# Kernel optimization log

Hardware: AMD Instinct MI355X
Metric: run time of the kernel (lower is better)

## Reference

```python
import jax, jax.numpy as jnp
import numpy as np

N_HEAD = 16
N_KV_HEAD = 8
HEAD_DIM = 128
N_EMBED = 2048
EPS = 1.1920929e-07  # torch default eps for fp32 rms_norm


def _apply_rotary_emb(x, cos, sin):
    # x: (B, T, H, D); cos/sin: (1, T, 1, D//2)  (nanochat-style half rotation)
    d = x.shape[-1] // 2
    x1, x2 = x[..., :d], x[..., d:]
    y1 = x1 * cos + x2 * sin
    y2 = -x1 * sin + x2 * cos
    return jnp.concatenate([y1, y2], axis=-1).astype(x.dtype)


def _rms_norm(x):
    return x * jax.lax.rsqrt(jnp.mean(jnp.square(x), axis=-1, keepdims=True) + EPS)


def setup_inputs() -> dict:
    key = jax.random.key(0)
    ks = jax.random.split(key, 5)
    B, T = 2, 2048
    kv_dim = N_KV_HEAD * HEAD_DIM
    x = jax.random.normal(ks[0], (B, T, N_EMBED), dtype=jnp.float32)
    w_attn = jax.random.normal(ks[1], (N_EMBED + 2 * kv_dim, N_EMBED), dtype=jnp.float32) * 0.02
    w_proj = jax.random.normal(ks[2], (N_EMBED, N_EMBED), dtype=jnp.float32) * 0.02
    # realistic RoPE tables
    half = HEAD_DIM // 2
    inv_freq = 1.0 / (10000.0 ** (jnp.arange(half, dtype=jnp.float32) / half))
    freqs = jnp.arange(T, dtype=jnp.float32)[:, None] * inv_freq[None, :]  # (T, half)
    cos = jnp.cos(freqs)[None, :, None, :]
    sin = jnp.sin(freqs)[None, :, None, :]
    return {"x": x, "w_attn": w_attn, "w_proj": w_proj, "cos": cos, "sin": sin}


def reference(x, w_attn, w_proj, cos, sin):
    B, T, C = x.shape
    kv_dim = N_KV_HEAD * HEAD_DIM
    qkv = jnp.einsum('btc,oc->bto', x, w_attn)  # (B, T, C + 2*kv_dim)
    q = qkv[..., :C].reshape(B, T, N_HEAD, HEAD_DIM)
    k = qkv[..., C:C + kv_dim].reshape(B, T, N_KV_HEAD, HEAD_DIM)
    v = qkv[..., C + kv_dim:].reshape(B, T, N_KV_HEAD, HEAD_DIM)
    q = _rms_norm(_apply_rotary_emb(q, cos, sin))
    k = _rms_norm(_apply_rotary_emb(k, cos, sin))
    # GQA: repeat kv heads to match query heads
    rep = N_HEAD // N_KV_HEAD
    k = jnp.repeat(k, rep, axis=2)  # (B, T, n_head, D)
    v = jnp.repeat(v, rep, axis=2)
    scale = 1.0 / jnp.sqrt(jnp.float32(HEAD_DIM))
    scores = jnp.einsum('bqhd,bkhd->bhqk', q, k) * scale  # (B, H, T, T)
    causal = jnp.tril(jnp.ones((T, T), dtype=bool))
    scores = jnp.where(causal[None, None], scores, jnp.finfo(scores.dtype).min)
    attn = jax.nn.softmax(scores, axis=-1)
    y = jnp.einsum('bhqk,bkhd->bqhd', attn, v).reshape(B, T, C)
    return jnp.einsum('btc,oc->bto', y, w_proj)
```

## Files before the change

### kernel.cpp

```cpp
#include <hip/hip_runtime.h>

#define B_ 2
#define T_ 2048
#define NH 16
#define NKV 8
#define HD 128
#define C_ 2048
#define KVD (NKV*HD)
#define QKVD (C_ + 2*KVD)
#define NTOK (B_*T_)

typedef __bf16 bf16_t;
typedef __bf16 bf16x4_t __attribute__((ext_vector_type(4)));
typedef __bf16 bf16x8_t __attribute__((ext_vector_type(8)));
typedef float f32x4_t __attribute__((ext_vector_type(4)));

__device__ __forceinline__ f32x4_t mfma16(bf16x8_t a, bf16x8_t b, f32x4_t c) {
  return __builtin_amdgcn_mfma_f32_16x16x32_bf16(a, b, c, 0, 0, 0);
}

#define GLDS16(gp, lp) __builtin_amdgcn_global_load_lds( \
    (const __attribute__((address_space(1))) void*)(gp), \
    (__attribute__((address_space(3))) void*)(lp), 16, 0, 0)

__global__ __launch_bounds__(256) void cvt_kernel(const float* __restrict__ src,
                                                  bf16_t* __restrict__ dst, int n) {
  int i = (blockIdx.x * 256 + threadIdx.x) * 4;
  if (i >= n) return;
  const float4 v = *(const float4*)(src + i);
  bf16x4_t o;
  o[0] = (bf16_t)v.x; o[1] = (bf16_t)v.y; o[2] = (bf16_t)v.z; o[3] = (bf16_t)v.w;
  *(bf16x4_t*)(dst + i) = o;
}

__global__ void gemm_nt(const bf16_t* __restrict__ A, const bf16_t* __restrict__ Bm,
                        float* __restrict__ C, int M, int N, int K) {
  __shared__ bf16_t As[128*32];
  __shared__ bf16_t Bs[128*32];
  int tid = threadIdx.x;
  int wave = tid >> 6, lane = tid & 63;
  int quad = lane >> 4, l16 = lane & 15;
  int wm = (wave >> 1) * 64, wn = (wave & 1) * 64;
  int bm = blockIdx.y * 128, bn = blockIdx.x * 128;
  int grow = wave * 32 + (lane >> 2);
  int gcol = (lane & 3) * 8;
  const bf16_t* pa = A + (size_t)(bm + grow) * K + gcol;
  const bf16_t* pb = Bm + (size_t)(bn + grow) * K + gcol;
  bf16_t* lA0 = &As[(wave * 32) * 32];
  bf16_t* lA1 = &As[(wave * 32 + 16) * 32];
  bf16_t* lB0 = &Bs[(wave * 32) * 32];
  bf16_t* lB1 = &Bs[(wave * 32 + 16) * 32];
  f32x4_t acc[4][4];
  #pragma unroll
  for (int i = 0; i < 4; i++)
    #pragma unroll
    for (int j = 0; j < 4; j++) acc[i][j] = (f32x4_t){0.f,0.f,0.f,0.f};
  for (int k0 = 0; k0 < K; k0 += 32) {
    __syncthreads();
    GLDS16(pa + k0, lA0);
    GLDS16(pa + (size_t)16 * K + k0, lA1);
    GLDS16(pb + k0, lB0);
    GLDS16(pb + (size_t)16 * K + k0, lB1);
    __syncthreads();
    bf16x8_t af[4], bfr[4];
    #pragma unroll
    for (int i = 0; i < 4; i++) {
      af[i]  = *(const bf16x8_t*)&As[(wm + i*16 + l16)*32 + quad*8];
      bfr[i] = *(const bf16x8_t*)&Bs[(wn + i*16 + l16)*32 + quad*8];
    }
    #pragma unroll
    for (int i = 0; i < 4; i++)
      #pragma unroll
      for (int j = 0; j < 4; j++)
        acc[i][j] = mfma16(af[i], bfr[j], acc[i][j]);
  }
  #pragma unroll
  for (int i = 0; i < 4; i++)
    #pragma unroll
    for (int j = 0; j < 4; j++) {
      int row0 = bm + wm + i*16 + quad*4;
      int col  = bn + wn + j*16 + l16;
      #pragma unroll
      for (int r = 0; r < 4; r++)
        C[(size_t)(row0 + r) * N + col] = acc[i][j][r];
    }
}

__global__ __launch_bounds__(256) void rope_norm_kernel(const float* __restrict__ qkv,
    const float* __restrict__ cosb, const float* __restrict__ sinb,
    bf16_t* __restrict__ qb, bf16_t* __restrict__ kb) {
  int token = blockIdx.y;
  int slot = blockIdx.x * 4 + (threadIdx.x >> 6);
  int lane = threadIdx.x & 63;
  int b = token >> 11, s = token & 2047;
  const float* row = qkv + (size_t)token * QKVD;
  int base_in = (slot < 16) ? slot * HD : C_ + (slot - 16) * HD;
  float x1 = row[base_in + lane];
  float x2 = row[base_in + 64 + lane];
  float c = cosb[s*64 + lane], sn = sinb[s*64 + lane];
  float y1 = x1*c + x2*sn;
  float y2 = x2*c - x1*sn;
  float ss = y1*y1 + y2*y2;
  ss += __shfl_xor(ss, 1);  ss += __shfl_xor(ss, 2);  ss += __shfl_xor(ss, 4);
  ss += __shfl_xor(ss, 8);  ss += __shfl_xor(ss, 16); ss += __shfl_xor(ss, 32);
  float r = rsqrtf(ss * (1.0f/128.0f) + 1.1920929e-07f);
  bf16_t* dst;
  if (slot < 16) {
    r *= 0.08838834764831845f * 1.4426950408889634f;
    dst = qb + ((size_t)(b*NH + slot) * T_ + s) * HD;
  } else {
    dst = kb + ((size_t)(b*NKV + (slot-16)) * T_ + s) * HD;
  }
  dst[lane]      = (bf16_t)(y1 * r);
  dst[lane + 64] = (bf16_t)(y2 * r);
}

__global__ __launch_bounds__(256) void transpose_v(const float* __restrict__ qkv,
                                                   bf16_t* __restrict__ vt) {
  __shared__ bf16_t TT[64*136];
  int bk = blockIdx.y;
  int b = bk >> 3, kv = bk & 7;
  int s0 = blockIdx.x * 64;
  int tid = threadIdx.x;
  int row = tid >> 2, c0 = (tid & 3) * 32;
  const float* src = qkv + (size_t)(b*T_ + s0 + row) * QKVD + C_ + KVD + kv*HD + c0;
  #pragma unroll
  for (int s4 = 0; s4 < 8; s4++) {
    float4 v = *(const float4*)(src + s4*4);
    bf16x4_t pk;
    pk[0] = (bf16_t)v.x; pk[1] = (bf16_t)v.y; pk[2] = (bf16_t)v.z; pk[3] = (bf16_t)v.w;
    *(bf16x4_t*)&TT[row*136 + c0 + s4*4] = pk;
  }
  __syncthreads();
  #pragma unroll
  for (int s2 = 0; s2 < 2; s2++) {
    int d = (tid >> 2) + s2*64;
    #pragma unroll
    for (int s = 0; s < 2; s++) {
      int g = (tid & 3) * 8 + s*32;
      bf16x8_t pk;
      #pragma unroll
      for (int e = 0; e < 8; e++) pk[e] = TT[(g + e)*136 + d];
      *(bf16x8_t*)(vt + ((size_t)bk * HD + d) * T_ + s0 + g) = pk;
    }
  }
}

__global__ __launch_bounds__(256, 2) void attn_kernel(const bf16_t* __restrict__ qb,
    const bf16_t* __restrict__ kb, const bf16_t* __restrict__ vt, bf16_t* __restrict__ yb) {
  __shared__ bf16_t Ks[64*136];
  __shared__ bf16_t Vs[128*72];
  __shared__ bf16_t Ps[4][16*72];
  int bh = blockIdx.y;
  int b = bh >> 4, h = bh & 15, kvh = h >> 1;
  int j = blockIdx.x;
  int tid = threadIdx.x, wave = tid >> 6, lane = tid & 63, quad = lane >> 4, l16 = lane & 15;
  const bf16_t* Qp = qb + (size_t)bh * T_ * HD;
  const bf16_t* Kp = kb + (size_t)(b*NKV + kvh) * T_ * HD;
  const bf16_t* Vt = vt + (size_t)(b*NKV + kvh) * HD * T_;

  int krow = tid >> 2, kc0 = (tid & 3) * 8;
  int vd = tid >> 1,  vc0 = (tid & 1) * 8;

  for (int ph = 0; ph < 2; ph++) {
    int qt = ph ? (31 - j) : j;
    int q0w = qt * 64 + wave * 16;
    bf16x8_t qf[4];
    #pragma unroll
    for (int kc = 0; kc < 4; kc++)
      qf[kc] = *(const bf16x8_t*)(Qp + (size_t)(q0w + l16) * HD + kc*32 + quad*8);

    float mrow = -1e30f, lrow = 0.f;
    f32x4_t o[8];
    #pragma unroll
    for (int mb = 0; mb < 8; mb++) o[mb] = (f32x4_t){0.f,0.f,0.f,0.f};

    int nkt = qt + 1;
    for (int kt = 0; kt < nkt; kt++) {
      int k0 = kt * 64;
      __syncthreads();
      {
        const bf16_t* src = Kp + (size_t)(k0 + krow) * HD + kc0;
        #pragma unroll
        for (int s = 0; s < 4; s++)
          *(bf16x8_t*)&Ks[krow*136 + kc0 + s*32] = *(const bf16x8_t*)(src + s*32);
      }
      {
        const bf16_t* src = Vt + (size_t)vd * T_ + k0 + vc0;
        #pragma unroll
        for (int s = 0; s < 4; s++)
          *(bf16x8_t*)&Vs[vd*72 + vc0 + s*16] = *(const bf16x8_t*)(src + s*16);
      }
      __syncthreads();

      f32x4_t sacc[4];
      #pragma unroll
      for (int mb = 0; mb < 4; mb++) sacc[mb] = (f32x4_t){0.f,0.f,0.f,0.f};
      #pragma unroll
      for (int mb = 0; mb < 4; mb++)
        #pragma unroll
        for (int kc = 0; kc < 4; kc++) {
          bf16x8_t kf = *(const bf16x8_t*)&Ks[(mb*16 + l16)*136 + kc*32 + quad*8];
          sacc[mb] = mfma16(kf, qf[kc], sacc[mb]);
        }
      if (kt == qt) {
        int rowl = wave*16 + l16;
        #pragma unroll
        for (int mb = 0; mb < 4; mb++)
          #pragma unroll
          for (int r = 0; r < 4; r++)
            if (mb*16 + quad*4 + r > rowl) sacc[mb][r] = -1e30f;
      }
      float mx = -1e30f;
      #pragma unroll
      for (int mb = 0; mb < 4; mb++)
        #pragma unroll
        for (int r = 0; r < 4; r++) mx = fmaxf(mx, sacc[mb][r]);
      mx = fmaxf(mx, __shfl_xor(mx, 16));
      mx = fmaxf(mx, __shfl_xor(mx, 32));
      float mnew = fmaxf(mrow, mx);
      float alpha = exp2f(mrow - mnew);
      mrow = mnew;
      float rs = 0.f;
      #pragma unroll
      for (int mb = 0; mb < 4; mb++)
        #pragma unroll
        for (int r = 0; r < 4; r++) {
          float p = exp2f(sacc[mb][r] - mnew);
          sacc[mb][r] = p;
          rs += p;
        }
      rs += __shfl_xor(rs, 16);
      rs += __shfl_xor(rs, 32);
      lrow = lrow * alpha + rs;
      #pragma unroll
      for (int mb = 0; mb < 8; mb++) o[mb] *= alpha;
      #pragma unroll
      for (int mb = 0; mb < 4; mb++) {
        bf16x4_t pk;
        pk[0] = (bf16_t)sacc[mb][0]; pk[1] = (bf16_t)sacc[mb][1];
        pk[2] = (bf16_t)sacc[mb][2]; pk[3] = (bf16_t)sacc[mb][3];
        *(bf16x4_t*)&Ps[wave][l16*72 + mb*16 + quad*4] = pk;
      }
      bf16x8_t pf[2];
      #pragma unroll
      for (int kc = 0; kc < 2; kc++)
        pf[kc] = *(const bf16x8_t*)&Ps[wave][l16*72 + kc*32 + quad*8];
      #pragma unroll
      for (int mb = 0; mb < 8; mb++)
        #pragma unroll
        for (int kc = 0; kc < 2; kc++) {
          bf16x8_t vf = *(const bf16x8_t*)&Vs[(mb*16 + l16)*72 + kc*32 + quad*8];
          o[mb] = mfma16(vf, pf[kc], o[mb]);
        }
    }
    __syncthreads();
    bf16_t* OLw = &Ks[wave * 2176];
    float invl = 1.0f / lrow;
    #pragma unroll
    for (int mb = 0; mb < 8; mb++) {
      bf16x4_t pk;
      pk[0] = (bf16_t)(o[mb][0] * invl); pk[1] = (bf16_t)(o[mb][1] * invl);
      pk[2] = (bf16_t)(o[mb][2] * invl); pk[3] = (bf16_t)(o[mb][3] * invl);
      *(bf16x4_t*)&OLw[l16*136 + mb*16 + quad*4] = pk;
    }
    int row = lane & 15, part = lane >> 4;
    int tok = qt*64 + wave*16 + row;
    bf16_t* dst = yb + ((size_t)(b*T_ + tok) * NH + h) * HD + part*32;
    #pragma unroll
    for (int jj = 0; jj < 4; jj++)
      *(bf16x8_t*)(dst + jj*8) = *(const bf16x8_t*)&OLw[row*136 + part*32 + jj*8];
  }
}

extern "C" void kernel_launch(void* const* d_in, const int* in_sizes, int n_in,
                              void* d_out, int out_size, void* d_ws, size_t ws_size,
                              hipStream_t stream) {
  const float* x      = (const float*)d_in[0];
  const float* w_attn = (const float*)d_in[1];
  const float* w_proj = (const float*)d_in[2];
  const float* cosb   = (const float*)d_in[3];
  const float* sinb   = (const float*)d_in[4];
  float* out = (float*)d_out;

  bf16_t* xb  = (bf16_t*)d_ws;
  bf16_t* wab = xb + 8388608;
  bf16_t* wpb = wab + 8388608;
  float*  qkv = (float*)(wpb + 4194304);
  bf16_t* qb  = (bf16_t*)(qkv + 16777216);
  bf16_t* kb  = qb + 8388608;
  bf16_t* vt  = kb + 4194304;
  bf16_t* yb  = vt + 4194304;

  cvt_kernel<<<8192, 256, 0, stream>>>(x, xb, 8388608);
  cvt_kernel<<<8192, 256, 0, stream>>>(w_attn, wab, 8388608);
  cvt_kernel<<<4096, 256, 0, stream>>>(w_proj, wpb, 4194304);

  gemm_nt<<<dim3(32, 32), 256, 0, stream>>>(xb, wab, qkv, NTOK, QKVD, C_);

  rope_norm_kernel<<<dim3(6, 4096), 256, 0, stream>>>(qkv, cosb, sinb, qb, kb);
  transpose_v<<<dim3(32, 16), 256, 0, stream>>>(qkv, vt);

  attn_kernel<<<dim3(16, 32), 256, 0, stream>>>(qb, kb, vt, yb);

  gemm_nt<<<dim3(16, 32), 256, 0, stream>>>(yb, wpb, out, NTOK, C_, C_);
}
```

Before: 359.6 us.

## Use 32x32 MFMA with 128-row query tiles, bf16 QKV output, and fused conversions

```diff
diff --git a/kernel.cpp b/kernel.cpp
--- a/kernel.cpp
+++ b/kernel.cpp
@@ -14,27 +14,42 @@
 typedef __bf16 bf16x4_t __attribute__((ext_vector_type(4)));
 typedef __bf16 bf16x8_t __attribute__((ext_vector_type(8)));
 typedef float f32x4_t __attribute__((ext_vector_type(4)));
+typedef float f32x16_t __attribute__((ext_vector_type(16)));
 
 __device__ __forceinline__ f32x4_t mfma16(bf16x8_t a, bf16x8_t b, f32x4_t c) {
   return __builtin_amdgcn_mfma_f32_16x16x32_bf16(a, b, c, 0, 0, 0);
+}
+__device__ __forceinline__ f32x16_t mfma32(bf16x8_t a, bf16x8_t b, f32x16_t c) {
+  return __builtin_amdgcn_mfma_f32_32x32x16_bf16(a, b, c, 0, 0, 0);
+}
+__device__ __forceinline__ f32x16_t zero16() {
+  f32x16_t z;
+  #pragma unroll
+  for (int i = 0; i < 16; i++) z[i] = 0.f;
+  return z;
 }
 
 #define GLDS16(gp, lp) __builtin_amdgcn_global_load_lds( \
     (const __attribute__((address_space(1))) void*)(gp), \
     (__attribute__((address_space(3))) void*)(lp), 16, 0, 0)
 
-__global__ __launch_bounds__(256) void cvt_kernel(const float* __restrict__ src,
-                                                  bf16_t* __restrict__ dst, int n) {
-  int i = (blockIdx.x * 256 + threadIdx.x) * 4;
-  if (i >= n) return;
-  const float4 v = *(const float4*)(src + i);
+__global__ __launch_bounds__(256) void cvt3_kernel(const float* __restrict__ s0, bf16_t* __restrict__ d0,
+                                                   const float* __restrict__ s1, bf16_t* __restrict__ d1,
+                                                   const float* __restrict__ s2, bf16_t* __restrict__ d2) {
+  int bid = blockIdx.x;
+  const float* s; bf16_t* d; int off;
+  if (bid < 8192)       { s = s0; d = d0; off = bid; }
+  else if (bid < 16384) { s = s1; d = d1; off = bid - 8192; }
+  else                  { s = s2; d = d2; off = bid - 16384; }
+  int i = (off * 256 + threadIdx.x) * 4;
+  const float4 v = *(const float4*)(s + i);
   bf16x4_t o;
   o[0] = (bf16_t)v.x; o[1] = (bf16_t)v.y; o[2] = (bf16_t)v.z; o[3] = (bf16_t)v.w;
-  *(bf16x4_t*)(dst + i) = o;
+  *(bf16x4_t*)(d + i) = o;
 }
 
 __global__ void gemm_nt(const bf16_t* __restrict__ A, const bf16_t* __restrict__ Bm,
-                        float* __restrict__ C, int M, int N, int K) {
+                        float* __restrict__ Cf, bf16_t* __restrict__ Cb, int M, int N, int K) {
   __shared__ bf16_t As[128*32];
   __shared__ bf16_t Bs[128*32];
   int tid = threadIdx.x;
@@ -74,29 +89,42 @@
       for (int j = 0; j < 4; j++)
         acc[i][j] = mfma16(af[i], bfr[j], acc[i][j]);
   }
-  #pragma unroll
-  for (int i = 0; i < 4; i++)
-    #pragma unroll
-    for (int j = 0; j < 4; j++) {
-      int row0 = bm + wm + i*16 + quad*4;
-      int col  = bn + wn + j*16 + l16;
-      #pragma unroll
-      for (int r = 0; r < 4; r++)
-        C[(size_t)(row0 + r) * N + col] = acc[i][j][r];
-    }
-}
-
-__global__ __launch_bounds__(256) void rope_norm_kernel(const float* __restrict__ qkv,
+  if (Cb) {
+    #pragma unroll
+    for (int i = 0; i < 4; i++)
+      #pragma unroll
+      for (int j = 0; j < 4; j++) {
+        int row0 = bm + wm + i*16 + quad*4;
+        int col  = bn + wn + j*16 + l16;
+        #pragma unroll
+        for (int r = 0; r < 4; r++)
+          Cb[(size_t)(row0 + r) * N + col] = (bf16_t)acc[i][j][r];
+      }
+  } else {
+    #pragma unroll
+    for (int i = 0; i < 4; i++)
+      #pragma unroll
+      for (int j = 0; j < 4; j++) {
+        int row0 = bm + wm + i*16 + quad*4;
+        int col  = bn + wn + j*16 + l16;
+        #pragma unroll
+        for (int r = 0; r < 4; r++)
+          Cf[(size_t)(row0 + r) * N + col] = acc[i][j][r];
+      }
+  }
+}
+
+__global__ __launch_bounds__(256) void rope_norm_kernel(const bf16_t* __restrict__ qkv,
     const float* __restrict__ cosb, const float* __restrict__ sinb,
     bf16_t* __restrict__ qb, bf16_t* __restrict__ kb) {
   int token = blockIdx.y;
   int slot = blockIdx.x * 4 + (threadIdx.x >> 6);
   int lane = threadIdx.x & 63;
   int b = token >> 11, s = token & 2047;
-  const float* row = qkv + (size_t)token * QKVD;
+  const bf16_t* row = qkv + (size_t)token * QKVD;
   int base_in = (slot < 16) ? slot * HD : C_ + (slot - 16) * HD;
-  float x1 = row[base_in + lane];
-  float x2 = row[base_in + 64 + lane];
+  float x1 = (float)row[base_in + lane];
+  float x2 = (float)row[base_in + 64 + lane];
   float c = cosb[s*64 + lane], sn = sinb[s*64 + lane];
   float y1 = x1*c + x2*sn;
   float y2 = x2*c - x1*sn;
@@ -115,7 +143,7 @@
   dst[lane + 64] = (bf16_t)(y2 * r);
 }
 
-__global__ __launch_bounds__(256) void transpose_v(const float* __restrict__ qkv,
+__global__ __launch_bounds__(256) void transpose_v(const bf16_t* __restrict__ qkv,
                                                    bf16_t* __restrict__ vt) {
   __shared__ bf16_t TT[64*136];
   int bk = blockIdx.y;
@@ -123,14 +151,10 @@
   int s0 = blockIdx.x * 64;
   int tid = threadIdx.x;
   int row = tid >> 2, c0 = (tid & 3) * 32;
-  const float* src = qkv + (size_t)(b*T_ + s0 + row) * QKVD + C_ + KVD + kv*HD + c0;
-  #pragma unroll
-  for (int s4 = 0; s4 < 8; s4++) {
-    float4 v = *(const float4*)(src + s4*4);
-    bf16x4_t pk;
-    pk[0] = (bf16_t)v.x; pk[1] = (bf16_t)v.y; pk[2] = (bf16_t)v.z; pk[3] = (bf16_t)v.w;
-    *(bf16x4_t*)&TT[row*136 + c0 + s4*4] = pk;
-  }
+  const bf16_t* src = qkv + (size_t)(b*T_ + s0 + row) * QKVD + C_ + KVD + kv*HD + c0;
+  #pragma unroll
+  for (int s4 = 0; s4 < 4; s4++)
+    *(bf16x8_t*)&TT[row*136 + c0 + s4*8] = *(const bf16x8_t*)(src + s4*8);
   __syncthreads();
   #pragma unroll
   for (int s2 = 0; s2 < 2; s2++) {
@@ -150,127 +174,130 @@
     const bf16_t* __restrict__ kb, const bf16_t* __restrict__ vt, bf16_t* __restrict__ yb) {
   __shared__ bf16_t Ks[64*136];
   __shared__ bf16_t Vs[128*72];
-  __shared__ bf16_t Ps[4][16*72];
-  int bh = blockIdx.y;
+  __shared__ bf16_t Ps[4][32*72];
+  int L = blockIdx.x;
+  int s = (L >> 8) & 1;
+  int bh = (L >> 3) & 31;
+  int qt = s ? (15 - 2*(L & 7)) : (2*(L & 7));
   int b = bh >> 4, h = bh & 15, kvh = h >> 1;
-  int j = blockIdx.x;
-  int tid = threadIdx.x, wave = tid >> 6, lane = tid & 63, quad = lane >> 4, l16 = lane & 15;
+  int tid = threadIdx.x, wave = tid >> 6, lane = tid & 63;
+  int l32 = lane & 31, half = lane >> 5;
   const bf16_t* Qp = qb + (size_t)bh * T_ * HD;
   const bf16_t* Kp = kb + (size_t)(b*NKV + kvh) * T_ * HD;
   const bf16_t* Vt = vt + (size_t)(b*NKV + kvh) * HD * T_;
 
-  int krow = tid >> 2, kc0 = (tid & 3) * 8;
-  int vd = tid >> 1,  vc0 = (tid & 1) * 8;
-
-  for (int ph = 0; ph < 2; ph++) {
-    int qt = ph ? (31 - j) : j;
-    int q0w = qt * 64 + wave * 16;
-    bf16x8_t qf[4];
+  int qrow = qt*128 + wave*32 + l32;
+  bf16x8_t qf[8];
+  #pragma unroll
+  for (int kc = 0; kc < 8; kc++)
+    qf[kc] = *(const bf16x8_t*)(Qp + (size_t)qrow * HD + kc*16 + half*8);
+
+  float mrow = -1e30f, lrow = 0.f;
+  f32x16_t o[4];
+  #pragma unroll
+  for (int mb = 0; mb < 4; mb++) o[mb] = zero16();
+
+  int krow = tid >> 2, kcb = (tid & 3) * 32;
+  int vd = tid >> 1,  vcb = (tid & 1) * 32;
+
+  int nkt = 2*qt + 2;
+  for (int kt = 0; kt < nkt; kt++) {
+    int k0 = kt * 64;
+    __syncthreads();
+    {
+      const bf16_t* src = Kp + (size_t)(k0 + krow) * HD + kcb;
+      #pragma unroll
+      for (int ss2 = 0; ss2 < 4; ss2++)
+        *(bf16x8_t*)&Ks[krow*136 + kcb + ss2*8] = *(const bf16x8_t*)(src + ss2*8);
+    }
+    {
+      const bf16_t* src = Vt + (size_t)vd * T_ + k0 + vcb;
+      #pragma unroll
+      for (int ss2 = 0; ss2 < 4; ss2++)
+        *(bf16x8_t*)&Vs[vd*72 + vcb + ss2*8] = *(const bf16x8_t*)(src + ss2*8);
+    }
+    __syncthreads();
+
+    f32x16_t sacc[2];
+    sacc[0] = zero16(); sacc[1] = zero16();
+    #pragma unroll
+    for (int kc = 0; kc < 8; kc++) {
+      #pragma unroll
+      for (int mb = 0; mb < 2; mb++) {
+        bf16x8_t kf = *(const bf16x8_t*)&Ks[(mb*32 + l32)*136 + kc*16 + half*8];
+        sacc[mb] = mfma32(kf, qf[kc], sacc[mb]);
+      }
+    }
+    if (k0 + 63 > qt*128 + wave*32) {
+      #pragma unroll
+      for (int mb = 0; mb < 2; mb++)
+        #pragma unroll
+        for (int r = 0; r < 16; r++) {
+          int key = k0 + mb*32 + (r&3) + 8*(r>>2) + 4*half;
+          if (key > qrow) sacc[mb][r] = -1e30f;
+        }
+    }
+    float mx = -1e30f;
+    #pragma unroll
+    for (int mb = 0; mb < 2; mb++)
+      #pragma unroll
+      for (int r = 0; r < 16; r++) mx = fmaxf(mx, sacc[mb][r]);
+    mx = fmaxf(mx, __shfl_xor(mx, 32));
+    float mnew = fmaxf(mrow, mx);
+    float alpha = exp2f(mrow - mnew);
+    mrow = mnew;
+    float rs = 0.f;
+    #pragma unroll
+    for (int mb = 0; mb < 2; mb++)
+      #pragma unroll
+      for (int r = 0; r < 16; r++) {
+        float p = exp2f(sacc[mb][r] - mnew);
+        sacc[mb][r] = p;
+        rs += p;
+      }
+    rs += __shfl_xor(rs, 32);
+    lrow = lrow * alpha + rs;
+    #pragma unroll
+    for (int mb = 0; mb < 4; mb++) o[mb] = o[mb] * alpha;
+    #pragma unroll
+    for (int mb = 0; mb < 2; mb++)
+      #pragma unroll
+      for (int rr = 0; rr < 4; rr++) {
+        bf16x4_t pk;
+        pk[0] = (bf16_t)sacc[mb][rr*4+0]; pk[1] = (bf16_t)sacc[mb][rr*4+1];
+        pk[2] = (bf16_t)sacc[mb][rr*4+2]; pk[3] = (bf16_t)sacc[mb][rr*4+3];
+        *(bf16x4_t*)&Ps[wave][l32*72 + mb*32 + rr*8 + half*4] = pk;
+      }
+    bf16x8_t pf[4];
     #pragma unroll
     for (int kc = 0; kc < 4; kc++)
-      qf[kc] = *(const bf16x8_t*)(Qp + (size_t)(q0w + l16) * HD + kc*32 + quad*8);
-
-    float mrow = -1e30f, lrow = 0.f;
-    f32x4_t o[8];
-    #pragma unroll
-    for (int mb = 0; mb < 8; mb++) o[mb] = (f32x4_t){0.f,0.f,0.f,0.f};
-
-    int nkt = qt + 1;
-    for (int kt = 0; kt < nkt; kt++) {
-      int k0 = kt * 64;
-      __syncthreads();
-      {
-        const bf16_t* src = Kp + (size_t)(k0 + krow) * HD + kc0;
-        #pragma unroll
-        for (int s = 0; s < 4; s++)
-          *(bf16x8_t*)&Ks[krow*136 + kc0 + s*32] = *(const bf16x8_t*)(src + s*32);
-      }
-      {
-        const bf16_t* src = Vt + (size_t)vd * T_ + k0 + vc0;
-        #pragma unroll
-        for (int s = 0; s < 4; s++)
-          *(bf16x8_t*)&Vs[vd*72 + vc0 + s*16] = *(const bf16x8_t*)(src + s*16);
-      }
-      __syncthreads();
-
-      f32x4_t sacc[4];
-      #pragma unroll
-      for (int mb = 0; mb < 4; mb++) sacc[mb] = (f32x4_t){0.f,0.f,0.f,0.f};
-      #pragma unroll
-      for (int mb = 0; mb < 4; mb++)
-        #pragma unroll
-        for (int kc = 0; kc < 4; kc++) {
-          bf16x8_t kf = *(const bf16x8_t*)&Ks[(mb*16 + l16)*136 + kc*32 + quad*8];
-          sacc[mb] = mfma16(kf, qf[kc], sacc[mb]);
-        }
-      if (kt == qt) {
-        int rowl = wave*16 + l16;
-        #pragma unroll
-        for (int mb = 0; mb < 4; mb++)
-          #pragma unroll
-          for (int r = 0; r < 4; r++)
-            if (mb*16 + quad*4 + r > rowl) sacc[mb][r] = -1e30f;
-      }
-      float mx = -1e30f;
-      #pragma unroll
-      for (int mb = 0; mb < 4; mb++)
-        #pragma unroll
-        for (int r = 0; r < 4; r++) mx = fmaxf(mx, sacc[mb][r]);
-      mx = fmaxf(mx, __shfl_xor(mx, 16));
-      mx = fmaxf(mx, __shfl_xor(mx, 32));
-      float mnew = fmaxf(mrow, mx);
-      float alpha = exp2f(mrow - mnew);
-      mrow = mnew;
-      float rs = 0.f;
-      #pragma unroll
-      for (int mb = 0; mb < 4; mb++)
-        #pragma unroll
-        for (int r = 0; r < 4; r++) {
-          float p = exp2f(sacc[mb][r] - mnew);
-          sacc[mb][r] = p;
-          rs += p;
-        }
-      rs += __shfl_xor(rs, 16);
-      rs += __shfl_xor(rs, 32);
-      lrow = lrow * alpha + rs;
-      #pragma unroll
-      for (int mb = 0; mb < 8; mb++) o[mb] *= alpha;
-      #pragma unroll
-      for (int mb = 0; mb < 4; mb++) {
-        bf16x4_t pk;
-        pk[0] = (bf16_t)sacc[mb][0]; pk[1] = (bf16_t)sacc[mb][1];
-        pk[2] = (bf16_t)sacc[mb][2]; pk[3] = (bf16_t)sacc[mb][3];
-        *(bf16x4_t*)&Ps[wave][l16*72 + mb*16 + quad*4] = pk;
-      }
-      bf16x8_t pf[2];
-      #pragma unroll
-      for (int kc = 0; kc < 2; kc++)
-        pf[kc] = *(const bf16x8_t*)&Ps[wave][l16*72 + kc*32 + quad*8];
-      #pragma unroll
-      for (int mb = 0; mb < 8; mb++)
-        #pragma unroll
-        for (int kc = 0; kc < 2; kc++) {
-          bf16x8_t vf = *(const bf16x8_t*)&Vs[(mb*16 + l16)*72 + kc*32 + quad*8];
-          o[mb] = mfma16(vf, pf[kc], o[mb]);
-        }
-    }
-    __syncthreads();
-    bf16_t* OLw = &Ks[wave * 2176];
-    float invl = 1.0f / lrow;
-    #pragma unroll
-    for (int mb = 0; mb < 8; mb++) {
+      pf[kc] = *(const bf16x8_t*)&Ps[wave][l32*72 + kc*16 + half*8];
+    #pragma unroll
+    for (int mb = 0; mb < 4; mb++)
+      #pragma unroll
+      for (int kc = 0; kc < 4; kc++) {
+        bf16x8_t vf = *(const bf16x8_t*)&Vs[(mb*32 + l32)*72 + kc*16 + half*8];
+        o[mb] = mfma32(vf, pf[kc], o[mb]);
+      }
+  }
+  __syncthreads();
+  bf16_t* OL = (wave < 2) ? &Ks[wave * 4352] : &Vs[(wave - 2) * 4352];
+  float invl = 1.0f / lrow;
+  #pragma unroll
+  for (int mb = 0; mb < 4; mb++)
+    #pragma unroll
+    for (int rr = 0; rr < 4; rr++) {
       bf16x4_t pk;
-      pk[0] = (bf16_t)(o[mb][0] * invl); pk[1] = (bf16_t)(o[mb][1] * invl);
-      pk[2] = (bf16_t)(o[mb][2] * invl); pk[3] = (bf16_t)(o[mb][3] * invl);
-      *(bf16x4_t*)&OLw[l16*136 + mb*16 + quad*4] = pk;
-    }
-    int row = lane & 15, part = lane >> 4;
-    int tok = qt*64 + wave*16 + row;
-    bf16_t* dst = yb + ((size_t)(b*T_ + tok) * NH + h) * HD + part*32;
-    #pragma unroll
-    for (int jj = 0; jj < 4; jj++)
-      *(bf16x8_t*)(dst + jj*8) = *(const bf16x8_t*)&OLw[row*136 + part*32 + jj*8];
-  }
+      pk[0] = (bf16_t)(o[mb][rr*4+0] * invl); pk[1] = (bf16_t)(o[mb][rr*4+1] * invl);
+      pk[2] = (bf16_t)(o[mb][rr*4+2] * invl); pk[3] = (bf16_t)(o[mb][rr*4+3] * invl);
+      *(bf16x4_t*)&OL[l32*136 + mb*32 + rr*8 + half*4] = pk;
+    }
+  int row = l32, seg = half;
+  int tok = qt*128 + wave*32 + row;
+  bf16_t* dst = yb + ((size_t)(b*T_ + tok) * NH + h) * HD + seg*64;
+  #pragma unroll
+  for (int j = 0; j < 8; j++)
+    *(bf16x8_t*)(dst + j*8) = *(const bf16x8_t*)&OL[row*136 + seg*64 + j*8];
 }
 
 extern "C" void kernel_launch(void* const* d_in, const int* in_sizes, int n_in,
@@ -283,25 +310,23 @@
   const float* sinb   = (const float*)d_in[4];
   float* out = (float*)d_out;
 
-  bf16_t* xb  = (bf16_t*)d_ws;
-  bf16_t* wab = xb + 8388608;
-  bf16_t* wpb = wab + 8388608;
-  float*  qkv = (float*)(wpb + 4194304);
-  bf16_t* qb  = (bf16_t*)(qkv + 16777216);
-  bf16_t* kb  = qb + 8388608;
-  bf16_t* vt  = kb + 4194304;
-  bf16_t* yb  = vt + 4194304;
-
-  cvt_kernel<<<8192, 256, 0, stream>>>(x, xb, 8388608);
-  cvt_kernel<<<8192, 256, 0, stream>>>(w_attn, wab, 8388608);
-  cvt_kernel<<<4096, 256, 0, stream>>>(w_proj, wpb, 4194304);
-
-  gemm_nt<<<dim3(32, 32), 256, 0, stream>>>(xb, wab, qkv, NTOK, QKVD, C_);
-
-  rope_norm_kernel<<<dim3(6, 4096), 256, 0, stream>>>(qkv, cosb, sinb, qb, kb);
-  transpose_v<<<dim3(32, 16), 256, 0, stream>>>(qkv, vt);
-
-  attn_kernel<<<dim3(16, 32), 256, 0, stream>>>(qb, kb, vt, yb);
-
-  gemm_nt<<<dim3(16, 32), 256, 0, stream>>>(yb, wpb, out, NTOK, C_, C_);
-}
+  bf16_t* xb   = (bf16_t*)d_ws;
+  bf16_t* wab  = xb + 8388608;
+  bf16_t* wpb  = wab + 8388608;
+  bf16_t* qkvb = wpb + 4194304;
+  bf16_t* qb   = qkvb + 16777216;
+  bf16_t* kb   = qb + 8388608;
+  bf16_t* vt   = kb + 4194304;
+  bf16_t* yb   = vt + 4194304;
+
+  cvt3_kernel<<<20480, 256, 0, stream>>>(x, xb, w_attn, wab, w_proj, wpb);
+
+  gemm_nt<<<dim3(32, 32), 256, 0, stream>>>(xb, wab, nullptr, qkvb, NTOK, QKVD, C_);
+
+  rope_norm_kernel<<<dim3(6, 4096), 256, 0, stream>>>(qkvb, cosb, sinb, qb, kb);
+  transpose_v<<<dim3(32, 16), 256, 0, stream>>>(qkvb, vt);
+
+  attn_kernel<<<512, 256, 0, stream>>>(qb, kb, vt, yb);
+
+  gemm_nt<<<dim3(16, 32), 256, 0, stream>>>(yb, wpb, out, nullptr, NTOK, C_, C_);
+}
```

New measurement: 353.9 us. About the same (-1.6%).
